# Performance work log

Hardware: AMD Instinct MI355X
Metric: run time of the kernel (lower is better)

## Reference

```python
import jax, jax.numpy as jnp
import numpy as np


def setup_inputs() -> dict:
    key = jax.random.key(0)
    k1, k2 = jax.random.split(key)
    B, C, H, W = 8, 32, 384, 384
    # probability-map-like predictions in [0, 1)
    pred = jax.random.uniform(k1, (B, C, H, W), dtype=jnp.float32)
    target = jax.random.randint(k2, (B, H, W), 0, C)  # int labels, all classes present w.h.p.
    return {"pred": pred, "target": target}


def reference(pred, target):
    """J-statistic loss (arXiv:1910.09783). reduction='none', weights=ones.

    Original computes, for each ci != ck:
      loss[b,ci,ck] = w[ci,ck] * log(0.5 + sum_hw pred[b,ci]*(phi[b,ci]-phi[b,ck])/2)
    where phi = one_hot(target)/n_i. The O(C^2) loop collapses to a single
    batched contraction S[b,i,k] = <pred[b,i], phi[b,k]> over spatial dims.
    """
    B, C, H, W = pred.shape
    t1h = jax.nn.one_hot(target, C, dtype=pred.dtype)          # (B,H,W,C)
    t1h = jnp.moveaxis(t1h, -1, 1)                             # (B,C,H,W)
    n_i = t1h.sum(axis=(-2, -1))[:, :, None, None]             # (B,C,1,1) class pixel counts
    phi = t1h / n_i                                            # normalized one-hot
    # S[b,i,k] = sum_hw pred[b,i]*phi[b,k]
    S = jnp.einsum('bihw,bkhw->bik', pred, phi)                # (B,C,C)
    diag = jnp.diagonal(S, axis1=1, axis2=2)                   # (B,C) = S[b,i,i]
    delta_sum = (diag[:, :, None] - S) * 0.5                   # sum_hw pred_i * (phi_i - phi_k)/2
    weights = jnp.ones((C, C), dtype=pred.dtype)
    loss = weights * jnp.log(0.5 + delta_sum)                  # (B,C,C)
    off_diag = 1.0 - jnp.eye(C, dtype=pred.dtype)              # skip ci == ck terms
    j = -(loss * off_diag).sum(axis=(-2, -1))                  # (B,)
    return j
```

## Files before the change

kernel.cpp:

```cpp
#include <hip/hip_runtime.h>


#define BB 8
#define CC 32
#define HW 147456
#define CHUNK_PX 1024
#define NCHUNK (HW / CHUNK_PX)

typedef __attribute__((ext_vector_type(8))) short short8;
typedef __attribute__((ext_vector_type(4))) float float4v;
typedef __attribute__((ext_vector_type(4))) unsigned uint4v;

__device__ __forceinline__ unsigned pk(float lo, float hi) {
    return __builtin_amdgcn_perm(__float_as_uint(hi), __float_as_uint(lo), 0x07060302u);
}
__device__ __forceinline__ unsigned oh2(int ta, int tb, int m) {
    return (ta == m ? 0x3F80u : 0u) | (tb == m ? 0x3F800000u : 0u);
}

__global__ __launch_bounds__(256, 4) void jloss_mfma(
    const float* __restrict__ pred,
    const int*   __restrict__ target,
    float*       __restrict__ T,
    float*       __restrict__ cnt)
{
    const int tid  = threadIdx.x;
    const int w    = tid >> 6;
    const int l    = tid & 63;
    const int quad = l >> 4;
    const int m    = l & 15;
    const int blk  = blockIdx.x;
    const int b    = blk / NCHUNK;
    const int chunk= blk % NCHUNK;

    const long pb_wave = (long)chunk * CHUNK_PX + w * 256;
    const float* predb = pred + (long)b * CC * HW;
    const int*   tgtb  = target + (long)b * HW;

    float4v acc00 = {0,0,0,0}, acc01 = {0,0,0,0};
    float4v acc10 = {0,0,0,0}, acc11 = {0,0,0,0};
    float4v accc0 = {0,0,0,0}, accc1 = {0,0,0,0};
    const short8 ONES = {0x3F80,0x3F80,0x3F80,0x3F80,0x3F80,0x3F80,0x3F80,0x3F80};

    #pragma unroll 2
    for (int ks = 0; ks < 8; ++ks) {
        const long po = pb_wave + ks * 32 + quad * 8;
        const float* p0 = predb + (long)m * HW + po;
        const float* p1 = p0 + (long)16 * HW;
        const float4 a0l = *(const float4*)p0;
        const float4 a0h = *(const float4*)(p0 + 4);
        const float4 a1l = *(const float4*)p1;
        const float4 a1h = *(const float4*)(p1 + 4);
        const int4 t0 = *(const int4*)(tgtb + po);
        const int4 t1 = *(const int4*)(tgtb + po + 4);

        union { short8 s; uint4v u; } A0, A1, B0, B1;
        A0.u[0] = pk(a0l.x, a0l.y); A0.u[1] = pk(a0l.z, a0l.w);
        A0.u[2] = pk(a0h.x, a0h.y); A0.u[3] = pk(a0h.z, a0h.w);
        A1.u[0] = pk(a1l.x, a1l.y); A1.u[1] = pk(a1l.z, a1l.w);
        A1.u[2] = pk(a1h.x, a1h.y); A1.u[3] = pk(a1h.z, a1h.w);
        B0.u[0] = oh2(t0.x, t0.y, m);      B0.u[1] = oh2(t0.z, t0.w, m);
        B0.u[2] = oh2(t1.x, t1.y, m);      B0.u[3] = oh2(t1.z, t1.w, m);
        const int m16 = m + 16;
        B1.u[0] = oh2(t0.x, t0.y, m16);    B1.u[1] = oh2(t0.z, t0.w, m16);
        B1.u[2] = oh2(t1.x, t1.y, m16);    B1.u[3] = oh2(t1.z, t1.w, m16);

        acc00 = __builtin_amdgcn_mfma_f32_16x16x32_bf16(A0.s, B0.s, acc00, 0, 0, 0);
        acc01 = __builtin_amdgcn_mfma_f32_16x16x32_bf16(A0.s, B1.s, acc01, 0, 0, 0);
        acc10 = __builtin_amdgcn_mfma_f32_16x16x32_bf16(A1.s, B0.s, acc10, 0, 0, 0);
        acc11 = __builtin_amdgcn_mfma_f32_16x16x32_bf16(A1.s, B1.s, acc11, 0, 0, 0);
        accc0 = __builtin_amdgcn_mfma_f32_16x16x32_bf16(ONES, B0.s, accc0, 0, 0, 0);
        accc1 = __builtin_amdgcn_mfma_f32_16x16x32_bf16(ONES, B1.s, accc1, 0, 0, 0);
    }

    __shared__ float red[4][CC][CC];
    __shared__ float redc[4][CC];
    #pragma unroll
    for (int r = 0; r < 4; ++r) {
        red[w][quad*4 + r     ][m     ] = acc00[r];
        red[w][quad*4 + r     ][m + 16] = acc01[r];
        red[w][quad*4 + r + 16][m     ] = acc10[r];
        red[w][quad*4 + r + 16][m + 16] = acc11[r];
    }
    if (quad == 0) {
        redc[w][m]      = accc0[0];
        redc[w][m + 16] = accc1[0];
    }
    __syncthreads();

    float* Tb = T + (long)b * CC * CC;
    const float* rp = &red[0][0][0];
    for (int j = tid; j < CC * CC; j += 256) {
        const float s = rp[j] + rp[1024 + j] + rp[2048 + j] + rp[3072 + j];
        atomicAdd(&Tb[j], s);
    }
    if (tid < CC)
        atomicAdd(&cnt[b * CC + tid],
                  redc[0][tid] + redc[1][tid] + redc[2][tid] + redc[3][tid]);
}

__global__ __launch_bounds__(256) void jloss_final(
    const float* __restrict__ T,
    const float* __restrict__ cnt,
    float*       __restrict__ out)
{
    const int b   = blockIdx.x;
    const int tid = threadIdx.x;
    __shared__ float diag_s[CC];
    __shared__ float inv_n[CC];
    __shared__ float wsum[4];

    const float* Tb = T + (long)b * CC * CC;
    const float* cb = cnt + b * CC;

    if (tid < CC) {
        const float inv = 1.0f / cb[tid];
        inv_n[tid]  = inv;
        diag_s[tid] = Tb[tid * CC + tid] * inv;
    }
    __syncthreads();

    float sum = 0.0f;
    for (int idx = tid; idx < CC * CC; idx += 256) {
        const int i = idx >> 5;
        const int k = idx & 31;
        if (i != k) {
            const float S = Tb[idx] * inv_n[k];
            sum += logf(0.5f + 0.5f * (diag_s[i] - S));
        }
    }
    #pragma unroll
    for (int off = 32; off > 0; off >>= 1) sum += __shfl_down(sum, off, 64);
    if ((tid & 63) == 0) wsum[tid >> 6] = sum;
    __syncthreads();
    if (tid == 0) out[b] = -(wsum[0] + wsum[1] + wsum[2] + wsum[3]);
}

extern "C" void kernel_launch(void* const* d_in, const int* in_sizes, int n_in,
                              void* d_out, int out_size, void* d_ws, size_t ws_size,
                              hipStream_t stream) {
    const float* pred   = (const float*)d_in[0];
    const int*   target = (const int*)d_in[1];
    float* out = (float*)d_out;

    float* T   = (float*)d_ws;
    float* cnt = (float*)d_ws + BB * CC * CC;

    hipMemsetAsync(d_ws, 0, (BB * CC * CC + BB * CC) * sizeof(float), stream);

    jloss_mfma <<<BB * NCHUNK, 256, 0, stream>>>(pred, target, T, cnt);
    jloss_final<<<BB, 256, 0, stream>>>(T, cnt, out);
}
```

Baseline: 222.5 us.

## Stage pred tiles into LDS via global_load_lds with smaller per-block chunks

Each block now covers 256 pixels instead of 1024. It copies all 32 channel rows into a padded LDS tile using coalesced 16-byte global_load_lds transfers, then builds the MFMA A operands from LDS. Before, each lane read strided per-channel global addresses directly. The LDS tile is reused for the cross-wave reduction buffers. The aim is better global-load coalescing and more blocks in flight, at the cost of four times more blocks issuing atomicAdds onto the same 8K output words, plus an extra barrier per block.

```diff
diff --git a/kernel.cpp b/kernel.cpp
--- a/kernel.cpp
+++ b/kernel.cpp
@@ -4,8 +4,9 @@
 #define BB 8
 #define CC 32
 #define HW 147456
-#define CHUNK_PX 1024
-#define NCHUNK (HW / CHUNK_PX)
+#define PX_BLK 256
+#define NCHUNK (HW / PX_BLK)
+#define STRIDE 258
 
 typedef __attribute__((ext_vector_type(8))) short short8;
 typedef __attribute__((ext_vector_type(4))) float float4v;
@@ -24,6 +25,8 @@
     float*       __restrict__ T,
     float*       __restrict__ cnt)
 {
+    __shared__ float tile[CC * STRIDE];
+
     const int tid  = threadIdx.x;
     const int w    = tid >> 6;
     const int l    = tid & 63;
@@ -33,32 +36,42 @@
     const int b    = blk / NCHUNK;
     const int chunk= blk % NCHUNK;
 
-    const long pb_wave = (long)chunk * CHUNK_PX + w * 256;
+    const long px0 = (long)chunk * PX_BLK;
     const float* predb = pred + (long)b * CC * HW;
     const int*   tgtb  = target + (long)b * HW;
+
+    #pragma unroll
+    for (int r = 0; r < 8; ++r) {
+        const int c = w * 8 + r;
+        const float* gp = predb + (long)c * HW + px0 + l * 4;
+        __builtin_amdgcn_global_load_lds(
+            (const __attribute__((address_space(1))) void*)gp,
+            (__attribute__((address_space(3))) void*)&tile[c * STRIDE + l * 4],
+            16, 0, 0);
+    }
+    __syncthreads();
 
     float4v acc00 = {0,0,0,0}, acc01 = {0,0,0,0};
     float4v acc10 = {0,0,0,0}, acc11 = {0,0,0,0};
     float4v accc0 = {0,0,0,0}, accc1 = {0,0,0,0};
     const short8 ONES = {0x3F80,0x3F80,0x3F80,0x3F80,0x3F80,0x3F80,0x3F80,0x3F80};
 
-    #pragma unroll 2
-    for (int ks = 0; ks < 8; ++ks) {
-        const long po = pb_wave + ks * 32 + quad * 8;
-        const float* p0 = predb + (long)m * HW + po;
-        const float* p1 = p0 + (long)16 * HW;
-        const float4 a0l = *(const float4*)p0;
-        const float4 a0h = *(const float4*)(p0 + 4);
-        const float4 a1l = *(const float4*)p1;
-        const float4 a1h = *(const float4*)(p1 + 4);
-        const int4 t0 = *(const int4*)(tgtb + po);
-        const int4 t1 = *(const int4*)(tgtb + po + 4);
+    #pragma unroll
+    for (int kk = 0; kk < 2; ++kk) {
+        const int ks   = w * 2 + kk;
+        const int base = ks * 32 + quad * 8;
+        const float2* r0 = (const float2*)&tile[m * STRIDE + base];
+        const float2* r1 = (const float2*)&tile[(m + 16) * STRIDE + base];
+        const float2 x0 = r0[0], x1 = r0[1], x2 = r0[2], x3 = r0[3];
+        const float2 y0 = r1[0], y1 = r1[1], y2 = r1[2], y3 = r1[3];
+        const int4 t0 = *(const int4*)(tgtb + px0 + base);
+        const int4 t1 = *(const int4*)(tgtb + px0 + base + 4);
 
         union { short8 s; uint4v u; } A0, A1, B0, B1;
-        A0.u[0] = pk(a0l.x, a0l.y); A0.u[1] = pk(a0l.z, a0l.w);
-        A0.u[2] = pk(a0h.x, a0h.y); A0.u[3] = pk(a0h.z, a0h.w);
-        A1.u[0] = pk(a1l.x, a1l.y); A1.u[1] = pk(a1l.z, a1l.w);
-        A1.u[2] = pk(a1h.x, a1h.y); A1.u[3] = pk(a1h.z, a1h.w);
+        A0.u[0] = pk(x0.x, x0.y); A0.u[1] = pk(x1.x, x1.y);
+        A0.u[2] = pk(x2.x, x2.y); A0.u[3] = pk(x3.x, x3.y);
+        A1.u[0] = pk(y0.x, y0.y); A1.u[1] = pk(y1.x, y1.y);
+        A1.u[2] = pk(y2.x, y2.y); A1.u[3] = pk(y3.x, y3.y);
         B0.u[0] = oh2(t0.x, t0.y, m);      B0.u[1] = oh2(t0.z, t0.w, m);
         B0.u[2] = oh2(t1.x, t1.y, m);      B0.u[3] = oh2(t1.z, t1.w, m);
         const int m16 = m + 16;
@@ -72,9 +85,10 @@
         accc0 = __builtin_amdgcn_mfma_f32_16x16x32_bf16(ONES, B0.s, accc0, 0, 0, 0);
         accc1 = __builtin_amdgcn_mfma_f32_16x16x32_bf16(ONES, B1.s, accc1, 0, 0, 0);
     }
+    __syncthreads();
 
-    __shared__ float red[4][CC][CC];
-    __shared__ float redc[4][CC];
+    float (*red)[CC][CC] = (float (*)[CC][CC])tile;
+    float* redc = tile + 4 * CC * CC;
     #pragma unroll
     for (int r = 0; r < 4; ++r) {
         red[w][quad*4 + r     ][m     ] = acc00[r];
@@ -83,8 +97,8 @@
         red[w][quad*4 + r + 16][m + 16] = acc11[r];
     }
     if (quad == 0) {
-        redc[w][m]      = accc0[0];
-        redc[w][m + 16] = accc1[0];
+        redc[w * CC + m]      = accc0[0];
+        redc[w * CC + m + 16] = accc1[0];
     }
     __syncthreads();
 
@@ -96,7 +110,7 @@
     }
     if (tid < CC)
         atomicAdd(&cnt[b * CC + tid],
-                  redc[0][tid] + redc[1][tid] + redc[2][tid] + redc[3][tid]);
+                  redc[tid] + redc[CC + tid] + redc[2*CC + tid] + redc[3*CC + tid]);
 }
 
 __global__ __launch_bounds__(256) void jloss_final(
```

Measured after the change: 236.8 us. +6.5%, slower.

## Split class counting into separate ballot kernel and shrink MFMA chunk size

Applied to the files above, without the earlier changes.

Drops the two ones-vector MFMAs from the main contraction kernel and computes the class pixel counts in a new kernel that uses wave ballots and popcounts. The MFMA kernel's chunk is halved, so it launches twice as many blocks, and its launch bound is raised to 6 waves. The goal is less MFMA work per block and more parallelism. The cost is a second full read of the target array, an extra launch, and twice as many atomicAdds into the 32x32 accumulators.

```diff
diff --git a/kernel.cpp b/kernel.cpp
--- a/kernel.cpp
+++ b/kernel.cpp
@@ -4,8 +4,10 @@
 #define BB 8
 #define CC 32
 #define HW 147456
-#define CHUNK_PX 1024
+#define CHUNK_PX 512
 #define NCHUNK (HW / CHUNK_PX)
+#define CNT_PX 4096
+#define NCNT (HW / CNT_PX)
 
 typedef __attribute__((ext_vector_type(8))) short short8;
 typedef __attribute__((ext_vector_type(4))) float float4v;
@@ -18,11 +20,10 @@
     return (ta == m ? 0x3F80u : 0u) | (tb == m ? 0x3F800000u : 0u);
 }
 
-__global__ __launch_bounds__(256, 4) void jloss_mfma(
+__global__ __launch_bounds__(256, 6) void jloss_mfma(
     const float* __restrict__ pred,
     const int*   __restrict__ target,
-    float*       __restrict__ T,
-    float*       __restrict__ cnt)
+    float*       __restrict__ T)
 {
     const int tid  = threadIdx.x;
     const int w    = tid >> 6;
@@ -33,26 +34,26 @@
     const int b    = blk / NCHUNK;
     const int chunk= blk % NCHUNK;
 
-    const long pb_wave = (long)chunk * CHUNK_PX + w * 256;
+    const long pb_wave = (long)chunk * CHUNK_PX + w * 128;
     const float* predb = pred + (long)b * CC * HW;
     const int*   tgtb  = target + (long)b * HW;
 
     float4v acc00 = {0,0,0,0}, acc01 = {0,0,0,0};
     float4v acc10 = {0,0,0,0}, acc11 = {0,0,0,0};
-    float4v accc0 = {0,0,0,0}, accc1 = {0,0,0,0};
-    const short8 ONES = {0x3F80,0x3F80,0x3F80,0x3F80,0x3F80,0x3F80,0x3F80,0x3F80};
 
-    #pragma unroll 2
-    for (int ks = 0; ks < 8; ++ks) {
-        const long po = pb_wave + ks * 32 + quad * 8;
-        const float* p0 = predb + (long)m * HW + po;
-        const float* p1 = p0 + (long)16 * HW;
-        const float4 a0l = *(const float4*)p0;
-        const float4 a0h = *(const float4*)(p0 + 4);
-        const float4 a1l = *(const float4*)p1;
-        const float4 a1h = *(const float4*)(p1 + 4);
-        const int4 t0 = *(const int4*)(tgtb + po);
-        const int4 t1 = *(const int4*)(tgtb + po + 4);
+    const float* p0 = predb + (long)m * HW + pb_wave + quad * 8;
+    const float* p1 = p0 + (long)16 * HW;
+    const int*   tp = tgtb + pb_wave + quad * 8;
+
+    #pragma unroll 1
+    for (int ks = 0; ks < 4; ++ks) {
+        const int o = ks * 32;
+        const float4 a0l = *(const float4*)(p0 + o);
+        const float4 a0h = *(const float4*)(p0 + o + 4);
+        const float4 a1l = *(const float4*)(p1 + o);
+        const float4 a1h = *(const float4*)(p1 + o + 4);
+        const int4 t0 = *(const int4*)(tp + o);
+        const int4 t1 = *(const int4*)(tp + o + 4);
 
         union { short8 s; uint4v u; } A0, A1, B0, B1;
         A0.u[0] = pk(a0l.x, a0l.y); A0.u[1] = pk(a0l.z, a0l.w);
@@ -69,22 +70,15 @@
         acc01 = __builtin_amdgcn_mfma_f32_16x16x32_bf16(A0.s, B1.s, acc01, 0, 0, 0);
         acc10 = __builtin_amdgcn_mfma_f32_16x16x32_bf16(A1.s, B0.s, acc10, 0, 0, 0);
         acc11 = __builtin_amdgcn_mfma_f32_16x16x32_bf16(A1.s, B1.s, acc11, 0, 0, 0);
-        accc0 = __builtin_amdgcn_mfma_f32_16x16x32_bf16(ONES, B0.s, accc0, 0, 0, 0);
-        accc1 = __builtin_amdgcn_mfma_f32_16x16x32_bf16(ONES, B1.s, accc1, 0, 0, 0);
     }
 
     __shared__ float red[4][CC][CC];
-    __shared__ float redc[4][CC];
     #pragma unroll
     for (int r = 0; r < 4; ++r) {
         red[w][quad*4 + r     ][m     ] = acc00[r];
         red[w][quad*4 + r     ][m + 16] = acc01[r];
         red[w][quad*4 + r + 16][m     ] = acc10[r];
         red[w][quad*4 + r + 16][m + 16] = acc11[r];
-    }
-    if (quad == 0) {
-        redc[w][m]      = accc0[0];
-        redc[w][m + 16] = accc1[0];
     }
     __syncthreads();
 
@@ -94,9 +88,35 @@
         const float s = rp[j] + rp[1024 + j] + rp[2048 + j] + rp[3072 + j];
         atomicAdd(&Tb[j], s);
     }
-    if (tid < CC)
-        atomicAdd(&cnt[b * CC + tid],
-                  redc[0][tid] + redc[1][tid] + redc[2][tid] + redc[3][tid]);
+}
+
+__global__ __launch_bounds__(256) void jloss_cnt(
+    const int* __restrict__ target,
+    float*     __restrict__ cnt)
+{
+    const int tid = threadIdx.x;
+    const int l   = tid & 63;
+    const int blk = blockIdx.x;
+    const int b   = blk / NCNT;
+    const int seg = blk % NCNT;
+    const int* tb = target + (long)b * HW + (long)seg * CNT_PX + tid * 4;
+
+    int c[CC];
+    #pragma unroll
+    for (int k = 0; k < CC; ++k) c[k] = 0;
+    #pragma unroll
+    for (int it = 0; it < CNT_PX / (256 * 4); ++it) {
+        const int4 t = *(const int4*)(tb + it * 1024);
+        #pragma unroll
+        for (int k = 0; k < CC; ++k)
+            c[k] += (int)__popcll(__ballot(t.x == k)) + (int)__popcll(__ballot(t.y == k))
+                  + (int)__popcll(__ballot(t.z == k)) + (int)__popcll(__ballot(t.w == k));
+    }
+    if (l == 0) {
+        #pragma unroll
+        for (int k = 0; k < CC; ++k)
+            atomicAdd(&cnt[b * CC + k], (float)c[k]);
+    }
 }
 
 __global__ __launch_bounds__(256) void jloss_final(
@@ -148,6 +168,7 @@
 
     hipMemsetAsync(d_ws, 0, (BB * CC * CC + BB * CC) * sizeof(float), stream);
 
-    jloss_mfma <<<BB * NCHUNK, 256, 0, stream>>>(pred, target, T, cnt);
+    jloss_cnt  <<<BB * NCNT,   256, 0, stream>>>(target, cnt);
+    jloss_mfma <<<BB * NCHUNK, 256, 0, stream>>>(pred, target, T);
     jloss_final<<<BB, 256, 0, stream>>>(T, cnt, out);
 }
```

After: 295.7 us. 1.33x slower.
